# Kernel optimization log

Hardware: AMD Instinct MI355X
Metric: run time of the kernel (lower is better)

Reference implementation:

```python
import jax, jax.numpy as jnp
import numpy as np

PI = float(np.pi)
QDIM = 64  # quantum_dim == state_dim == 2**num_qubits


def setup_inputs() -> dict:
    key = jax.random.key(0)
    ks = jax.random.split(key, 8)
    E, Q = 512, QDIM
    s = 1.0 / np.sqrt(E)
    return {
        "features": jax.random.normal(ks[0], (32, 4096, E), dtype=jnp.float32),
        "W_real": jax.random.normal(ks[1], (E, Q), dtype=jnp.float32) * s,
        "b_real": jnp.zeros((Q,), dtype=jnp.float32),
        "W_imag": jax.random.normal(ks[2], (E, Q), dtype=jnp.float32) * s,
        "b_imag": jnp.zeros((Q,), dtype=jnp.float32),
        "W_p1": jax.random.normal(ks[3], (E, Q), dtype=jnp.float32) * s,
        "b_p1": jnp.zeros((Q,), dtype=jnp.float32),
        "W_p2": jax.random.normal(ks[4], (Q, Q), dtype=jnp.float32) * (1.0 / np.sqrt(Q)),
        "b_p2": jnp.zeros((Q,), dtype=jnp.float32),
        "op_params": jax.random.normal(ks[5], (Q,), dtype=jnp.float32),
    }


def hermitian_operator(p):
    # operator_real: eye with diag replaced by sigmoid(p); off-diag [i,j] = p_i * p_j (symmetric)
    R = p[:, None] * p[None, :]
    d = jnp.arange(QDIM)
    R = R.at[d, d].set(jax.nn.sigmoid(p))
    # operator_imag: [i,j] = p_i - p_j (antisymmetric, zero diag)
    I = p[:, None] - p[None, :]
    return R, I


def reference(features, W_real, b_real, W_imag, b_imag, W_p1, b_p1, W_p2, b_p2, op_params):
    # --- QuantumStateEncoder ---
    r = jnp.tanh(features @ W_real + b_real)              # [B,S,Q]
    im = jnp.tanh(features @ W_imag + b_imag)             # [B,S,Q]
    phases = jnp.tanh(jnp.tanh(features @ W_p1 + b_p1) @ W_p2 + b_p2) * PI
    cr, ci = jnp.cos(phases), jnp.sin(phases)
    rp = r * cr - im * ci
    ip = r * ci + im * cr
    norm = jnp.sqrt(jnp.sum(rp * rp + ip * ip, axis=-1, keepdims=True) + 1e-12)
    rn = rp / norm
    inn = ip / norm
    # --- QuantumOperator (hermitian) ---
    R, I = hermitian_operator(op_params)
    out_r = rn @ R - inn @ I
    out_i = rn @ I + inn @ R
    return out_r, out_i, phases
```

## Files before the change

kernel.cpp:

```cpp
#include <hip/hip_runtime.h>
#include <math.h>

#define PI_F 3.14159265358979323846f

typedef __attribute__((ext_vector_type(8))) short  short8;
typedef __attribute__((ext_vector_type(4))) float  floatx4;

constexpr int E = 512;
constexpr int Q = 64;
constexpr int NCHUNK = E / 32;
constexpr int WS_B_ENTRIES = NCHUNK * 12 * 64;
constexpr int WS_P2_OFF = WS_B_ENTRIES;

__device__ __forceinline__ unsigned short bf16_rne(float x) {
    unsigned u = __float_as_uint(x);
    unsigned r = u + 0x7fffu + ((u >> 16) & 1u);
    return (unsigned short)(r >> 16);
}

__device__ __forceinline__ void split_bf16_8(const float* v, short8& hi, short8& lo) {
    #pragma unroll
    for (int j = 0; j < 8; ++j) {
        unsigned u  = __float_as_uint(v[j]);
        unsigned rh = (u + 0x7fffu + ((u >> 16) & 1u)) & 0xffff0000u;
        hi[j] = (short)(rh >> 16);
        float res = v[j] - __uint_as_float(rh);
        lo[j] = (short)bf16_rne(res);
    }
}

__device__ __forceinline__ float tanh_fast(float x) {
    const float xc = fminf(fmaxf(x, -15.f), 15.f);
    const float e  = __expf(2.f * xc);
    return (e - 1.f) / (e + 1.f);
}

__global__ void prep_weights(const float* __restrict__ Wr, const float* __restrict__ Wi,
                             const float* __restrict__ Wp1, const float* __restrict__ Wp2,
                             short* __restrict__ ws)
{
    const int e = blockIdx.x * 256 + threadIdx.x;
    const float* W;
    int kbase, n;
    if (e < WS_B_ENTRIES) {
        const int L = e & 63;
        const int f = e >> 6;
        const int tt = f & 3;
        const int g  = f >> 2;
        const int m  = g % 3, c = g / 3;
        W = (m == 0) ? Wr : (m == 1) ? Wi : Wp1;
        n     = tt * 16 + (L & 15);
        kbase = c * 32 + (L >> 4) * 8;
    } else {
        const int e2 = e - WS_B_ENTRIES;
        const int L  = e2 & 63;
        const int tt = (e2 >> 6) & 3;
        const int c2 = e2 >> 8;
        W = Wp2;
        n     = tt * 16 + (L & 15);
        kbase = c2 * 32 + (L >> 4) * 8;
    }
    short8 frag;
    #pragma unroll
    for (int j = 0; j < 8; ++j)
        frag[j] = (short)bf16_rne(W[(kbase + j) * Q + n]);
    *(short8*)(ws + (size_t)e * 8) = frag;
}

__global__ __launch_bounds__(256, 3)
void qi_mfma(const float* __restrict__ feat, const short* __restrict__ wsb,
             const float* __restrict__ br,  const float* __restrict__ bi,
             const float* __restrict__ bp1, const float* __restrict__ bp2,
             const float* __restrict__ op_p,
             float* __restrict__ out, long long nrows)
{
    __shared__ float Tp[4][16][68];

    const int tid = threadIdx.x;
    const int L   = tid & 63;
    const int w   = tid >> 6;
    const int l15 = L & 15;
    const int q4  = L >> 4;
    const long long rowBase = (long long)blockIdx.x * 64 + w * 16;

    const float* aptr = feat + (rowBase + l15) * (long long)E + q4 * 8;
    const short8* wfrag = (const short8*)wsb;

    floatx4 acc[12];
    #pragma unroll
    for (int t = 0; t < 12; ++t) acc[t] = (floatx4){0.f, 0.f, 0.f, 0.f};

    for (int c = 0; c < NCHUNK; ++c) {
        float av[8];
        {
            const floatx4 a0 = *(const floatx4*)(aptr + c * 32);
            const floatx4 a1 = *(const floatx4*)(aptr + c * 32 + 4);
            #pragma unroll
            for (int j = 0; j < 4; ++j) { av[j] = a0[j]; av[4 + j] = a1[j]; }
        }
        short8 ah, al;
        split_bf16_8(av, ah, al);

        const size_t cb = (size_t)(c * 12) * 64 + L;
        #pragma unroll
        for (int mt = 0; mt < 12; ++mt) {
            const short8 bf = wfrag[cb + (size_t)mt * 64];
            acc[mt] = __builtin_amdgcn_mfma_f32_16x16x32_bf16(ah, bf, acc[mt], 0, 0, 0);
            acc[mt] = __builtin_amdgcn_mfma_f32_16x16x32_bf16(al, bf, acc[mt], 0, 0, 0);
        }
    }

    float brv[4], biv[4], bp1v[4], bp2v[4], pv[4], dcv[4];
    #pragma unroll
    for (int t = 0; t < 4; ++t) {
        const int colv = t * 16 + l15;
        brv[t] = br[colv]; biv[t] = bi[colv]; bp1v[t] = bp1[colv]; bp2v[t] = bp2[colv];
        const float p = op_p[colv];
        pv[t]  = p;
        dcv[t] = 1.f / (1.f + __expf(-p)) - p * p;
    }

    float rv[4][4], iv[4][4];
    #pragma unroll
    for (int t = 0; t < 4; ++t)
        #pragma unroll
        for (int g = 0; g < 4; ++g) {
            rv[t][g] = tanh_fast(acc[t][g]     + brv[t]);
            iv[t][g] = tanh_fast(acc[4 + t][g] + biv[t]);
            Tp[w][q4 * 4 + g][t * 16 + l15] = tanh_fast(acc[8 + t][g] + bp1v[t]);
        }
    __syncthreads();

    floatx4 accp2[4];
    #pragma unroll
    for (int t = 0; t < 4; ++t) accp2[t] = (floatx4){0.f, 0.f, 0.f, 0.f};
    #pragma unroll
    for (int c2 = 0; c2 < 2; ++c2) {
        float tv[8];
        {
            const floatx4 t0 = *(const floatx4*)&Tp[w][l15][c2 * 32 + q4 * 8];
            const floatx4 t1 = *(const floatx4*)&Tp[w][l15][c2 * 32 + q4 * 8 + 4];
            #pragma unroll
            for (int j = 0; j < 4; ++j) { tv[j] = t0[j]; tv[4 + j] = t1[j]; }
        }
        short8 th, tl;
        split_bf16_8(tv, th, tl);
        #pragma unroll
        for (int tt = 0; tt < 4; ++tt) {
            const short8 bf = wfrag[(size_t)(WS_P2_OFF + (c2 * 4 + tt) * 64 + L)];
            accp2[tt] = __builtin_amdgcn_mfma_f32_16x16x32_bf16(th, bf, accp2[tt], 0, 0, 0);
            accp2[tt] = __builtin_amdgcn_mfma_f32_16x16x32_bf16(tl, bf, accp2[tt], 0, 0, 0);
        }
    }

    float* __restrict__ outR = out;
    float* __restrict__ outI = out +       nrows * Q;
    float* __restrict__ outP = out + 2LL * nrows * Q;

    float rp[4][4], ip[4][4];
    #pragma unroll
    for (int t = 0; t < 4; ++t)
        #pragma unroll
        for (int g = 0; g < 4; ++g) {
            const float ph = tanh_fast(accp2[t][g] + bp2v[t]) * PI_F;
            const long long row = rowBase + q4 * 4 + g;
            outP[row * Q + t * 16 + l15] = ph;
            const float si = __sinf(ph), co = __cosf(ph);
            rp[t][g] = rv[t][g] * co - iv[t][g] * si;
            ip[t][g] = rv[t][g] * si + iv[t][g] * co;
        }

    #pragma unroll
    for (int g = 0; g < 4; ++g) {
        float n2 = 0.f;
        #pragma unroll
        for (int t = 0; t < 4; ++t) n2 += rp[t][g] * rp[t][g] + ip[t][g] * ip[t][g];
        #pragma unroll
        for (int off = 1; off <= 8; off <<= 1) n2 += __shfl_xor(n2, off);
        const float inv = 1.f / sqrtf(n2 + 1e-12f);

        float dR = 0.f, dI = 0.f, sR = 0.f, sI = 0.f;
        #pragma unroll
        for (int t = 0; t < 4; ++t) {
            rp[t][g] *= inv; ip[t][g] *= inv;
            dR += rp[t][g] * pv[t];  dI += ip[t][g] * pv[t];
            sR += rp[t][g];          sI += ip[t][g];
        }
        #pragma unroll
        for (int off = 1; off <= 8; off <<= 1) {
            dR += __shfl_xor(dR, off); dI += __shfl_xor(dI, off);
            sR += __shfl_xor(sR, off); sI += __shfl_xor(sI, off);
        }

        const long long row = rowBase + q4 * 4 + g;
        #pragma unroll
        for (int t = 0; t < 4; ++t) {
            const long long o = row * Q + t * 16 + l15;
            outR[o] = dR * pv[t] + rp[t][g] * dcv[t] - dI + sI * pv[t];
            outI[o] = dR - sR * pv[t] + ip[t][g] * dcv[t] + dI * pv[t];
        }
    }
}

extern "C" void kernel_launch(void* const* d_in, const int* in_sizes, int n_in,
                              void* d_out, int out_size, void* d_ws, size_t ws_size,
                              hipStream_t stream) {
    const float* feat = (const float*)d_in[0];
    const float* Wr   = (const float*)d_in[1];
    const float* br   = (const float*)d_in[2];
    const float* Wi   = (const float*)d_in[3];
    const float* bi   = (const float*)d_in[4];
    const float* Wp1  = (const float*)d_in[5];
    const float* bp1  = (const float*)d_in[6];
    const float* Wp2  = (const float*)d_in[7];
    const float* bp2  = (const float*)d_in[8];
    const float* opp  = (const float*)d_in[9];

    short* ws = (short*)d_ws;

    const long long nrows = (long long)in_sizes[0] / E;
    const int blocks = (int)(nrows / 64);

    hipLaunchKernelGGL(prep_weights, dim3((WS_B_ENTRIES + 512) / 256), dim3(256), 0, stream,
                       Wr, Wi, Wp1, Wp2, ws);
    hipLaunchKernelGGL(qi_mfma, dim3(blocks), dim3(256), 0, stream,
                       feat, ws, br, bi, bp1, bp2, opp, (float*)d_out, nrows);
}
```

Baseline: 452.8 us.

## Double-buffer weight chunks in LDS via async global_load_lds and prefetch features

Weight fragments for each K-chunk are now copied into a double-buffered LDS region with async global-to-LDS loads, shared by all four waves instead of each wave reading them from global memory. Feature rows for the next chunk are prefetched into registers while the current chunk's MFMAs run. The LDS buffer is unioned with the phase scratch array, and the occupancy hint is raised to four blocks. This adds a block-wide barrier every chunk, which may limit overlap.

After: 424.8 us. -6.2%, faster.

```diff
diff --git a/kernel.cpp b/kernel.cpp
--- a/kernel.cpp
+++ b/kernel.cpp
@@ -11,6 +11,7 @@
 constexpr int NCHUNK = E / 32;
 constexpr int WS_B_ENTRIES = NCHUNK * 12 * 64;
 constexpr int WS_P2_OFF = WS_B_ENTRIES;
+constexpr int CHUNK_BYTES = 12 * 64 * 16;
 
 __device__ __forceinline__ unsigned short bf16_rne(float x) {
     unsigned u = __float_as_uint(x);
@@ -33,6 +34,12 @@
     const float xc = fminf(fmaxf(x, -15.f), 15.f);
     const float e  = __expf(2.f * xc);
     return (e - 1.f) / (e + 1.f);
+}
+
+__device__ __forceinline__ void async_copy16(const void* g, void* l) {
+    __builtin_amdgcn_global_load_lds(
+        (const __attribute__((address_space(1))) unsigned int*)g,
+        (__attribute__((address_space(3))) unsigned int*)l, 16, 0, 0);
 }
 
 __global__ void prep_weights(const float* __restrict__ Wr, const float* __restrict__ Wi,
@@ -67,47 +74,72 @@
     *(short8*)(ws + (size_t)e * 8) = frag;
 }
 
-__global__ __launch_bounds__(256, 3)
+__global__ __launch_bounds__(256, 4)
 void qi_mfma(const float* __restrict__ feat, const short* __restrict__ wsb,
              const float* __restrict__ br,  const float* __restrict__ bi,
              const float* __restrict__ bp1, const float* __restrict__ bp2,
              const float* __restrict__ op_p,
              float* __restrict__ out, long long nrows)
 {
-    __shared__ float Tp[4][16][68];
+    __shared__ alignas(16) union {
+        short wbuf[2][CHUNK_BYTES / 2];
+        float tp[4][16][68];
+    } sh;
 
     const int tid = threadIdx.x;
     const int L   = tid & 63;
-    const int w   = tid >> 6;
+    const int wv  = tid >> 6;
     const int l15 = L & 15;
     const int q4  = L >> 4;
-    const long long rowBase = (long long)blockIdx.x * 64 + w * 16;
+    const long long rowBase = (long long)blockIdx.x * 64 + wv * 16;
 
     const float* aptr = feat + (rowBase + l15) * (long long)E + q4 * 8;
-    const short8* wfrag = (const short8*)wsb;
+
+    {
+        const char* g = (const char*)wsb + (size_t)tid * 16;
+        char*       l = (char*)sh.wbuf[0] + (size_t)tid * 16;
+        #pragma unroll
+        for (int r = 0; r < 3; ++r) async_copy16(g + r * 4096, l + r * 4096);
+    }
+    floatx4 a0 = *(const floatx4*)aptr;
+    floatx4 a1 = *(const floatx4*)(aptr + 4);
 
     floatx4 acc[12];
     #pragma unroll
     for (int t = 0; t < 12; ++t) acc[t] = (floatx4){0.f, 0.f, 0.f, 0.f};
 
+    __syncthreads();
+
+    int cur = 0;
     for (int c = 0; c < NCHUNK; ++c) {
+        floatx4 n0, n1;
+        const bool has_next = (c + 1 < NCHUNK);
+        if (has_next) {
+            const char* g = (const char*)wsb + (size_t)(c + 1) * CHUNK_BYTES + (size_t)tid * 16;
+            char*       l = (char*)sh.wbuf[cur ^ 1] + (size_t)tid * 16;
+            #pragma unroll
+            for (int r = 0; r < 3; ++r) async_copy16(g + r * 4096, l + r * 4096);
+            n0 = *(const floatx4*)(aptr + (c + 1) * 32);
+            n1 = *(const floatx4*)(aptr + (c + 1) * 32 + 4);
+        }
+
         float av[8];
-        {
-            const floatx4 a0 = *(const floatx4*)(aptr + c * 32);
-            const floatx4 a1 = *(const floatx4*)(aptr + c * 32 + 4);
-            #pragma unroll
-            for (int j = 0; j < 4; ++j) { av[j] = a0[j]; av[4 + j] = a1[j]; }
-        }
+        #pragma unroll
+        for (int j = 0; j < 4; ++j) { av[j] = a0[j]; av[4 + j] = a1[j]; }
         short8 ah, al;
         split_bf16_8(av, ah, al);
 
-        const size_t cb = (size_t)(c * 12) * 64 + L;
+        const short8* wl = (const short8*)sh.wbuf[cur];
         #pragma unroll
         for (int mt = 0; mt < 12; ++mt) {
-            const short8 bf = wfrag[cb + (size_t)mt * 64];
+            const short8 bf = wl[mt * 64 + L];
             acc[mt] = __builtin_amdgcn_mfma_f32_16x16x32_bf16(ah, bf, acc[mt], 0, 0, 0);
             acc[mt] = __builtin_amdgcn_mfma_f32_16x16x32_bf16(al, bf, acc[mt], 0, 0, 0);
         }
+
+        __syncthreads();
+        if (has_next) { a0 = n0; a1 = n1; }
+        cur ^= 1;
     }
 
     float brv[4], biv[4], bp1v[4], bp2v[4], pv[4], dcv[4];
@@ -127,10 +159,11 @@
         for (int g = 0; g < 4; ++g) {
             rv[t][g] = tanh_fast(acc[t][g]     + brv[t]);
             iv[t][g] = tanh_fast(acc[4 + t][g] + biv[t]);
-            Tp[w][q4 * 4 + g][t * 16 + l15] = tanh_fast(acc[8 + t][g] + bp1v[t]);
+            sh.tp[wv][q4 * 4 + g][t * 16 + l15] = tanh_fast(acc[8 + t][g] + bp1v[t]);
         }
     __syncthreads();
 
+    const short8* wfrag = (const short8*)wsb;
     floatx4 accp2[4];
     #pragma unroll
     for (int t = 0; t < 4; ++t) accp2[t] = (floatx4){0.f, 0.f, 0.f, 0.f};
@@ -138,8 +171,8 @@
     for (int c2 = 0; c2 < 2; ++c2) {
         float tv[8];
         {
-            const floatx4 t0 = *(const floatx4*)&Tp[w][l15][c2 * 32 + q4 * 8];
-            const floatx4 t1 = *(const floatx4*)&Tp[w][l15][c2 * 32 + q4 * 8 + 4];
+            const floatx4 t0 = *(const floatx4*)&sh.tp[wv][l15][c2 * 32 + q4 * 8];
+            const floatx4 t1 = *(const floatx4*)&sh.tp[wv][l15][c2 * 32 + q4 * 8 + 4];
             #pragma unroll
             for (int j = 0; j < 4; ++j) { tv[j] = t0[j]; tv[4 + j] = t1[j]; }
         }
```
